# Kernel optimization log

Measured on AMD Instinct MI355X. Metric: run time of the kernel, lower is better.

## Reference

```python
import jax, jax.numpy as jnp
from jax import lax
import numpy as np

B, S, T = 512, 1024, 64  # batch, seq_len, tag_vocab_size


def setup_inputs() -> dict:
    key = jax.random.key(0)
    k1, k2, k3, k4 = jax.random.split(key, 4)
    tags = jax.random.randint(k1, (B, S), 0, T)
    # sequences sorted by length descending, as the original slicing scheme assumes
    lengths = jnp.sort(jax.random.randint(k2, (B,), 1, S + 1))[::-1]
    mask = jnp.arange(S)[None, :] < lengths[:, None]  # [B,S] bool
    emit_score = jax.random.normal(k3, (B, S, T), dtype=jnp.float32)
    transition = jax.random.normal(k4, (T, T), dtype=jnp.float32)
    return {"tags": tags, "mask": mask, "emit_score": emit_score, "transition": transition}


def reference(tags, mask, emit_score, transition):
    maskf = mask.astype(emit_score.dtype)
    # gold-path score: emission at gold tags + transition between consecutive gold tags
    score = jnp.take_along_axis(emit_score, tags[:, :, None], axis=2)[..., 0]  # [B,S]
    score = score.at[:, 1:].add(transition[tags[:, :-1], tags[:, 1:]])
    total_score = (score * maskf).sum(axis=1)  # [B]

    # forward algorithm (logsumexp-semiring scan over time)
    def step(d, inputs):
        emit_i, mask_i = inputs  # [B,T], [B]
        # log_sum[b, t_prev, t_cur] = d[b,t_prev] + transition[t_prev,t_cur] + emit_i[b,t_cur]
        cand = jax.nn.logsumexp(d[:, :, None] + transition[None, :, :] + emit_i[:, None, :], axis=1)
        d = jnp.where(mask_i[:, None], cand, d)  # finished sequences keep their alpha
        return d, None

    d0 = emit_score[:, 0]  # [B,T]
    emits_t = jnp.swapaxes(emit_score, 0, 1)[1:]  # [S-1,B,T]
    masks_t = mask.T[1:]  # [S-1,B]
    d, _ = lax.scan(step, d0, (emits_t, masks_t))
    log_z = jax.nn.logsumexp(d, axis=1)  # [B]
    return -(total_score - log_z)
```

## Files before the change

### kernel.cpp

```cpp
#include <hip/hip_runtime.h>
#include <stdint.h>

#define NB 512
#define SL 1024
#define NT 64

typedef float v4f __attribute__((ext_vector_type(4)));

__device__ __forceinline__ float wave_max6(float v) {
    #pragma unroll
    for (int off = 32; off >= 1; off >>= 1)
        v = fmaxf(v, __shfl_xor(v, off, 64));
    return v;
}
__device__ __forceinline__ float wave_sum_f(float v) {
    #pragma unroll
    for (int off = 32; off >= 1; off >>= 1)
        v += __shfl_xor(v, off, 64);
    return v;
}

__device__ __forceinline__ uint32_t bf16_rne(float x) {
    uint32_t u = __float_as_uint(x);
    return (u + 0x7fffu + ((u >> 16) & 1u)) >> 16;
}

__device__ __forceinline__ void dot2bf(float& acc, uint32_t a, uint32_t b) {
    asm("v_dot2_f32_bf16 %0, %1, %2, %0" : "+v"(acc) : "v"(a), "v"(b));
}

__global__ void __launch_bounds__(64) crf_fused_kernel(
    const int* __restrict__ tags, const void* __restrict__ mask,
    const float* __restrict__ emit, const float* __restrict__ trans,
    float* __restrict__ out)
{
    const int b = blockIdx.x;
    const int lane = threadIdx.x;
    const float* erow = emit + (size_t)b * SL * NT;
    const int* trow = tags + b * SL;

    const unsigned char* mb = (const unsigned char*)mask;
    const bool mask_is_i32 = ((mb[1] | mb[2] | mb[3]) == 0);

    float acc = 0.f; int cnt = 0;
    #pragma unroll
    for (int j = 0; j < 16; ++j) {
        const int i = lane + 64 * j;
        const int mk = mask_is_i32 ? (((const int*)mask)[(size_t)b * SL + i] != 0)
                                   : (mb[(size_t)b * SL + i] != 0);
        if (mk) {
            const int tg = trow[i];
            float val = erow[(size_t)i * NT + tg];
            if (i > 0) val += trans[trow[i - 1] * NT + tg];
            acc += val; cnt += 1;
        }
    }
    #pragma unroll
    for (int off = 32; off >= 1; off >>= 1) {
        acc += __shfl_xor(acc, off, 64);
        cnt += __shfl_xor(cnt, off, 64);
    }
    const float ts = acc;
    const int len = cnt;

    uint32_t Epk[NT / 2];
    #pragma unroll
    for (int m = 0; m < NT / 2; ++m) {
        uint32_t lo = bf16_rne(__expf(trans[(2 * m + 0) * NT + lane]));
        uint32_t hi = bf16_rne(__expf(trans[(2 * m + 1) * NT + lane]));
        Epk[m] = lo | (hi << 16);
    }

    __shared__ __align__(16) uint16_t vbuf16[NT];

    float d0 = erow[lane];
    float m0 = wave_max6(d0);
    float v = __expf(d0 - m0);
    float logacc = m0;

#define STEP(EX)                                                           \
    {                                                                      \
        vbuf16[lane] = (uint16_t)bf16_rne(v);                              \
        __builtin_amdgcn_wave_barrier();                                   \
        float a0 = 0.f, a1 = 0.f, a2 = 0.f, a3 = 0.f;                      \
        float a4 = 0.f, a5 = 0.f, a6 = 0.f, a7 = 0.f;                      \
        const uint4* vb = (const uint4*)vbuf16;                            \
        _Pragma("unroll")                                                  \
        for (int r = 0; r < 8; r += 2) {                                   \
            uint4 q0 = vb[r];                                              \
            uint4 q1 = vb[r + 1];                                          \
            dot2bf(a0, q0.x, Epk[4 * r + 0]);                              \
            dot2bf(a1, q0.y, Epk[4 * r + 1]);                              \
            dot2bf(a2, q0.z, Epk[4 * r + 2]);                              \
            dot2bf(a3, q0.w, Epk[4 * r + 3]);                              \
            dot2bf(a4, q1.x, Epk[4 * r + 4]);                              \
            dot2bf(a5, q1.y, Epk[4 * r + 5]);                              \
            dot2bf(a6, q1.z, Epk[4 * r + 6]);                              \
            dot2bf(a7, q1.w, Epk[4 * r + 7]);                              \
        }                                                                  \
        float h = ((a0 + a1) + (a2 + a3)) + ((a4 + a5) + (a6 + a7));       \
        v = h * (EX);                                                      \
    }

    const int nstep = len - 1;
    const int ngrp = nstep >> 2;
    int i = 1;

    v4f emq;
    if (ngrp > 0) {
        emq.x = erow[(i + 0) * NT + lane];
        emq.y = erow[(i + 1) * NT + lane];
        emq.z = erow[(i + 2) * NT + lane];
        emq.w = erow[(i + 3) * NT + lane];
    }
    for (int g = 0; g < ngrp; ++g) {
        float ex0 = __expf(emq.x), ex1 = __expf(emq.y);
        float ex2 = __expf(emq.z), ex3 = __expf(emq.w);
        const int ip = i + 4;
        if (g + 1 < ngrp) {
            emq.x = erow[(ip + 0) * NT + lane];
            emq.y = erow[(ip + 1) * NT + lane];
            emq.z = erow[(ip + 2) * NT + lane];
            emq.w = erow[(ip + 3) * NT + lane];
        }
        STEP(ex0)
        STEP(ex1)
        STEP(ex2)
        STEP(ex3)
        {
            uint32_t sb = __builtin_amdgcn_readfirstlane(__float_as_uint(v));
            int ex = (int)((sb >> 23) & 0xffu);
            v *= __uint_as_float((uint32_t)(254 - ex) << 23);
            logacc += (float)(ex - 127) * 0.69314718055994530942f;
        }
        i += 4;
    }
    for (; i < len; ++i) {
        float e = __expf(erow[i * NT + lane]);
        STEP(e)
    }
#undef STEP

    float sum = wave_sum_f(v);
    float log_z = logacc + __logf(sum);
    if (lane == 0) out[b] = -(ts - log_z);
}

extern "C" void kernel_launch(void* const* d_in, const int* in_sizes, int n_in,
                              void* d_out, int out_size, void* d_ws, size_t ws_size,
                              hipStream_t stream) {
    (void)in_sizes; (void)n_in; (void)out_size; (void)d_ws; (void)ws_size;
    const int*   tags  = (const int*)d_in[0];
    const void*  mask  = d_in[1];
    const float* emit  = (const float*)d_in[2];
    const float* trans = (const float*)d_in[3];
    float* out = (float*)d_out;

    crf_fused_kernel<<<dim3(NB), dim3(64), 0, stream>>>(tags, mask, emit, trans, out);
}
```

Baseline: 388.8 us.

## Replace LDS broadcast of alpha vector with DPP row rotations and bpermute

```diff
diff --git a/kernel.cpp b/kernel.cpp
--- a/kernel.cpp
+++ b/kernel.cpp
@@ -27,6 +27,30 @@
 
 __device__ __forceinline__ void dot2bf(float& acc, uint32_t a, uint32_t b) {
     asm("v_dot2_f32_bf16 %0, %1, %2, %0" : "+v"(acc) : "v"(a), "v"(b));
+}
+__device__ __forceinline__ float dot2bf3(uint32_t a, uint32_t b, float c) {
+    float d;
+    asm("v_dot2_f32_bf16 %0, %1, %2, %3" : "=v"(d) : "v"(a), "v"(b), "v"(c));
+    return d;
+}
+
+__device__ __forceinline__ uint32_t cvtpk_bf16(float lo, float hi) {
+    uint32_t r;
+    asm("v_cvt_pk_bf16_f32 %0, %1, %2" : "=v"(r) : "v"(lo), "v"(hi));
+    return r;
+}
+
+#define ROR1 0x121
+#define ROR2 0x122
+#define ROR4 0x124
+#define ROR8 0x128
+template <int CTRL>
+__device__ __forceinline__ uint32_t dpp_u(uint32_t x) {
+    return (uint32_t)__builtin_amdgcn_mov_dpp((int)x, CTRL, 0xf, 0xf, true);
+}
+
+__device__ __forceinline__ float bperm_f(int addr, float x) {
+    return __int_as_float(__builtin_amdgcn_ds_bpermute(addr, __float_as_int(x)));
 }
 
 __global__ void __launch_bounds__(64) crf_fused_kernel(
@@ -63,43 +87,80 @@
     const float ts = acc;
     const int len = cnt;
 
-    uint32_t Epk[NT / 2];
-    #pragma unroll
-    for (int m = 0; m < NT / 2; ++m) {
-        uint32_t lo = bf16_rne(__expf(trans[(2 * m + 0) * NT + lane]));
-        uint32_t hi = bf16_rne(__expf(trans[(2 * m + 1) * NT + lane]));
-        Epk[m] = lo | (hi << 16);
-    }
-
-    __shared__ __align__(16) uint16_t vbuf16[NT];
+    uint32_t idx = (uint32_t)lane;
+    uint32_t i1 = dpp_u<ROR1>(idx);
+    uint32_t wIdx[8];
+    wIdx[0] = idx | (i1 << 16);
+    wIdx[1] = dpp_u<ROR2>(wIdx[0]);
+    wIdx[2] = dpp_u<ROR4>(wIdx[0]);
+    wIdx[3] = dpp_u<ROR4>(wIdx[1]);
+    wIdx[4] = dpp_u<ROR8>(wIdx[0]);
+    wIdx[5] = dpp_u<ROR8>(wIdx[1]);
+    wIdx[6] = dpp_u<ROR8>(wIdx[2]);
+    wIdx[7] = dpp_u<ROR8>(wIdx[3]);
+
+    uint32_t EpkR[4][8];
+    #pragma unroll
+    for (int k = 0; k < 4; ++k) {
+        const int col = lane ^ (k << 4);
+        #pragma unroll
+        for (int j = 0; j < 8; ++j) {
+            const int lo = (int)(wIdx[j] & 0xffffu);
+            const int hi = (int)(wIdx[j] >> 16);
+            const uint32_t el = bf16_rne(__expf(trans[lo * NT + col]));
+            const uint32_t eh = bf16_rne(__expf(trans[hi * NT + col]));
+            EpkR[k][j] = el | (eh << 16);
+        }
+    }
+
+    const int a16 = (lane ^ 16) << 2;
+    const int a32 = (lane ^ 32) << 2;
+    const int a48 = (lane ^ 48) << 2;
+    const float fzero = 0.0f;
 
     float d0 = erow[lane];
     float m0 = wave_max6(d0);
     float v = __expf(d0 - m0);
     float logacc = m0;
 
-#define STEP(EX)                                                           \
-    {                                                                      \
-        vbuf16[lane] = (uint16_t)bf16_rne(v);                              \
-        __builtin_amdgcn_wave_barrier();                                   \
-        float a0 = 0.f, a1 = 0.f, a2 = 0.f, a3 = 0.f;                      \
-        float a4 = 0.f, a5 = 0.f, a6 = 0.f, a7 = 0.f;                      \
-        const uint4* vb = (const uint4*)vbuf16;                            \
-        _Pragma("unroll")                                                  \
-        for (int r = 0; r < 8; r += 2) {                                   \
-            uint4 q0 = vb[r];                                              \
-            uint4 q1 = vb[r + 1];                                          \
-            dot2bf(a0, q0.x, Epk[4 * r + 0]);                              \
-            dot2bf(a1, q0.y, Epk[4 * r + 1]);                              \
-            dot2bf(a2, q0.z, Epk[4 * r + 2]);                              \
-            dot2bf(a3, q0.w, Epk[4 * r + 3]);                              \
-            dot2bf(a4, q1.x, Epk[4 * r + 4]);                              \
-            dot2bf(a5, q1.y, Epk[4 * r + 5]);                              \
-            dot2bf(a6, q1.z, Epk[4 * r + 6]);                              \
-            dot2bf(a7, q1.w, Epk[4 * r + 7]);                              \
-        }                                                                  \
-        float h = ((a0 + a1) + (a2 + a3)) + ((a4 + a5) + (a6 + a7));       \
-        v = h * (EX);                                                      \
+#define STEP(EX)                                                            \
+    {                                                                       \
+        const uint32_t n1 = dpp_u<ROR1>(__float_as_uint(v));                \
+        const uint32_t w0 = cvtpk_bf16(v, __uint_as_float(n1));             \
+        const uint32_t w1 = dpp_u<ROR2>(w0);                                \
+        const uint32_t w2 = dpp_u<ROR4>(w0);                                \
+        const uint32_t w3 = dpp_u<ROR4>(w1);                                \
+        const uint32_t w4 = dpp_u<ROR8>(w0);                                \
+        const uint32_t w5 = dpp_u<ROR8>(w1);                                \
+        const uint32_t w6 = dpp_u<ROR8>(w2);                                \
+        const uint32_t w7 = dpp_u<ROR8>(w3);                                \
+        float a0 = dot2bf3(w0, EpkR[0][0], fzero);                          \
+        float a1 = dot2bf3(w0, EpkR[1][0], fzero);                          \
+        float a2 = dot2bf3(w0, EpkR[2][0], fzero);                          \
+        float a3 = dot2bf3(w0, EpkR[3][0], fzero);                          \
+        dot2bf(a0, w1, EpkR[0][1]); dot2bf(a1, w1, EpkR[1][1]);             \
+        dot2bf(a2, w1, EpkR[2][1]); dot2bf(a3, w1, EpkR[3][1]);             \
+        dot2bf(a0, w2, EpkR[0][2]); dot2bf(a1, w2, EpkR[1][2]);             \
+        dot2bf(a2, w2, EpkR[2][2]); dot2bf(a3, w2, EpkR[3][2]);             \
+        dot2bf(a0, w3, EpkR[0][3]); dot2bf(a1, w3, EpkR[1][3]);             \
+        dot2bf(a2, w3, EpkR[2][3]); dot2bf(a3, w3, EpkR[3][3]);             \
+        float b0 = dot2bf3(w4, EpkR[0][4], fzero);                          \
+        float b1 = dot2bf3(w4, EpkR[1][4], fzero);                          \
+        float b2 = dot2bf3(w4, EpkR[2][4], fzero);                          \
+        float b3 = dot2bf3(w4, EpkR[3][4], fzero);                          \
+        dot2bf(b0, w5, EpkR[0][5]); dot2bf(b1, w5, EpkR[1][5]);             \
+        dot2bf(b2, w5, EpkR[2][5]); dot2bf(b3, w5, EpkR[3][5]);             \
+        dot2bf(b0, w6, EpkR[0][6]); dot2bf(b1, w6, EpkR[1][6]);             \
+        dot2bf(b2, w6, EpkR[2][6]); dot2bf(b3, w6, EpkR[3][6]);             \
+        dot2bf(b0, w7, EpkR[0][7]); dot2bf(b1, w7, EpkR[1][7]);             \
+        dot2bf(b2, w7, EpkR[2][7]); dot2bf(b3, w7, EpkR[3][7]);             \
+        const float acc1 = a1 + b1;                                         \
+        const float acc2 = a2 + b2;                                         \
+        const float acc3 = a3 + b3;                                         \
+        const float x1 = bperm_f(a16, acc1);                                \
+        const float x2 = bperm_f(a32, acc2);                                \
+        const float x3 = bperm_f(a48, acc3);                                \
+        v = (((a0 + b0) + x1) + (x2 + x3)) * (EX);                          \
     }
 
     const int nstep = len - 1;
```

New measurement: 359.2 us. -7.6%, faster.

## Batch 16 sequences per wave and run forward recursion with MFMA

Applied to the files above, without the earlier changes.

```diff
diff --git a/kernel.cpp b/kernel.cpp
--- a/kernel.cpp
+++ b/kernel.cpp
@@ -4,146 +4,214 @@
 #define NB 512
 #define SL 1024
 #define NT 64
-
-typedef float v4f __attribute__((ext_vector_type(4)));
-
-__device__ __forceinline__ float wave_max6(float v) {
-    #pragma unroll
-    for (int off = 32; off >= 1; off >>= 1)
-        v = fmaxf(v, __shfl_xor(v, off, 64));
-    return v;
-}
-__device__ __forceinline__ float wave_sum_f(float v) {
-    #pragma unroll
-    for (int off = 32; off >= 1; off >>= 1)
-        v += __shfl_xor(v, off, 64);
-    return v;
-}
+#define BPB 16
+
+typedef __attribute__((ext_vector_type(8))) short bf16x8;
+typedef __attribute__((ext_vector_type(4))) float f32x4;
+typedef __attribute__((ext_vector_type(4))) unsigned int u32x4;
 
 __device__ __forceinline__ uint32_t bf16_rne(float x) {
     uint32_t u = __float_as_uint(x);
     return (u + 0x7fffu + ((u >> 16) & 1u)) >> 16;
 }
-
-__device__ __forceinline__ void dot2bf(float& acc, uint32_t a, uint32_t b) {
-    asm("v_dot2_f32_bf16 %0, %1, %2, %0" : "+v"(acc) : "v"(a), "v"(b));
-}
-
-__global__ void __launch_bounds__(64) crf_fused_kernel(
+__device__ __forceinline__ uint32_t cvtpk_bf16(float lo, float hi) {
+    uint32_t r;
+    asm("v_cvt_pk_bf16_f32 %0, %1, %2" : "=v"(r) : "v"(lo), "v"(hi));
+    return r;
+}
+__device__ __forceinline__ void plswap16_f(float& a, float& b) {
+    asm("v_permlane16_swap_b32 %0, %1" : "+v"(a), "+v"(b));
+}
+__device__ __forceinline__ void plswap32_f(float& a, float& b) {
+    asm("v_permlane32_swap_b32 %0, %1" : "+v"(a), "+v"(b));
+}
+__device__ __forceinline__ void plswap16_i(int& a, int& b) {
+    asm("v_permlane16_swap_b32 %0, %1" : "+v"(a), "+v"(b));
+}
+__device__ __forceinline__ void plswap32_i(int& a, int& b) {
+    asm("v_permlane32_swap_b32 %0, %1" : "+v"(a), "+v"(b));
+}
+
+__device__ __forceinline__ f32x4 mfma_bf16(const u32x4& a, const u32x4& b, const f32x4& c) {
+    union U { u32x4 u; bf16x8 s; };
+    U ua; ua.u = a;
+    U ub; ub.u = b;
+    return __builtin_amdgcn_mfma_f32_16x16x32_bf16(ua.s, ub.s, c, 0, 0, 0);
+}
+
+__global__ void __launch_bounds__(64) crf_mfma_kernel(
     const int* __restrict__ tags, const void* __restrict__ mask,
     const float* __restrict__ emit, const float* __restrict__ trans,
     float* __restrict__ out)
 {
-    const int b = blockIdx.x;
+    const int b0 = blockIdx.x * BPB;
     const int lane = threadIdx.x;
-    const float* erow = emit + (size_t)b * SL * NT;
-    const int* trow = tags + b * SL;
+    const int q = lane >> 4;
+    const int n = lane & 15;
+    const int bb = b0 + n;
+
+    const int* trow = tags + (size_t)bb * SL;
+    const float* erow = emit + (size_t)bb * SL * NT;
 
     const unsigned char* mb = (const unsigned char*)mask;
-    const bool mask_is_i32 = ((mb[1] | mb[2] | mb[3]) == 0);
-
-    float acc = 0.f; int cnt = 0;
+    const bool m32 = ((mb[1] | mb[2] | mb[3]) == 0);
+
+    float acc = 0.f;
+    int cnt = 0;
+    const int i0 = q * (SL / 4);
+    #pragma unroll 8
+    for (int jj = 0; jj < SL / 4; ++jj) {
+        const int i = i0 + jj;
+        const int mk = m32 ? (((const int*)mask)[(size_t)bb * SL + i] != 0)
+                           : (mb[(size_t)bb * SL + i] != 0);
+        const int tg = trow[i];
+        float val = erow[(size_t)i * NT + tg];
+        if (i > 0) val += trans[trow[i - 1] * NT + tg];
+        acc += mk ? val : 0.f;
+        cnt += mk;
+    }
+    {
+        float pa = acc, pb = acc;
+        plswap16_f(pa, pb); acc = pa + pb;
+        pa = acc; pb = acc;
+        plswap32_f(pa, pb); acc = pa + pb;
+        int ca = cnt, cb = cnt;
+        plswap16_i(ca, cb); cnt = ca + cb;
+        ca = cnt; cb = cnt;
+        plswap32_i(ca, cb); cnt = ca + cb;
+    }
+    const float tsn = acc;
+    const int fin = cnt - 1;
+    const int lmax = __shfl(cnt, 0, 64);
+    const int last = lmax - 1;
+
+    u32x4 Afr[4][2];
     #pragma unroll
-    for (int j = 0; j < 16; ++j) {
-        const int i = lane + 64 * j;
-        const int mk = mask_is_i32 ? (((const int*)mask)[(size_t)b * SL + i] != 0)
-                                   : (mb[(size_t)b * SL + i] != 0);
-        if (mk) {
-            const int tg = trow[i];
-            float val = erow[(size_t)i * NT + tg];
-            if (i > 0) val += trans[trow[i - 1] * NT + tg];
-            acc += val; cnt += 1;
-        }
-    }
+    for (int T = 0; T < 4; ++T) {
+        #pragma unroll
+        for (int kt = 0; kt < 2; ++kt) {
+            uint32_t wv[4];
+            #pragma unroll
+            for (int w = 0; w < 4; ++w) {
+                const int p0 = 16 * (2 * kt + (w >> 1)) + 4 * q + 2 * (w & 1);
+                const int m = 16 * T + n;
+                const uint32_t lo = bf16_rne(__expf(trans[p0 * NT + m]));
+                const uint32_t hi = bf16_rne(__expf(trans[(p0 + 1) * NT + m]));
+                wv[w] = lo | (hi << 16);
+            }
+            Afr[T][kt].x = wv[0]; Afr[T][kt].y = wv[1];
+            Afr[T][kt].z = wv[2]; Afr[T][kt].w = wv[3];
+        }
+    }
+
+    const float* ep = erow + 4 * q;
+    f32x4 d[4];
     #pragma unroll
-    for (int off = 32; off >= 1; off >>= 1) {
-        acc += __shfl_xor(acc, off, 64);
-        cnt += __shfl_xor(cnt, off, 64);
-    }
-    const float ts = acc;
-    const int len = cnt;
-
-    uint32_t Epk[NT / 2];
-    #pragma unroll
-    for (int m = 0; m < NT / 2; ++m) {
-        uint32_t lo = bf16_rne(__expf(trans[(2 * m + 0) * NT + lane]));
-        uint32_t hi = bf16_rne(__expf(trans[(2 * m + 1) * NT + lane]));
-        Epk[m] = lo | (hi << 16);
-    }
-
-    __shared__ __align__(16) uint16_t vbuf16[NT];
-
-    float d0 = erow[lane];
-    float m0 = wave_max6(d0);
-    float v = __expf(d0 - m0);
-    float logacc = m0;
-
-#define STEP(EX)                                                           \
-    {                                                                      \
-        vbuf16[lane] = (uint16_t)bf16_rne(v);                              \
-        __builtin_amdgcn_wave_barrier();                                   \
-        float a0 = 0.f, a1 = 0.f, a2 = 0.f, a3 = 0.f;                      \
-        float a4 = 0.f, a5 = 0.f, a6 = 0.f, a7 = 0.f;                      \
-        const uint4* vb = (const uint4*)vbuf16;                            \
-        _Pragma("unroll")                                                  \
-        for (int r = 0; r < 8; r += 2) {                                   \
-            uint4 q0 = vb[r];                                              \
-            uint4 q1 = vb[r + 1];                                          \
-            dot2bf(a0, q0.x, Epk[4 * r + 0]);                              \
-            dot2bf(a1, q0.y, Epk[4 * r + 1]);                              \
-            dot2bf(a2, q0.z, Epk[4 * r + 2]);                              \
-            dot2bf(a3, q0.w, Epk[4 * r + 3]);                              \
-            dot2bf(a4, q1.x, Epk[4 * r + 4]);                              \
-            dot2bf(a5, q1.y, Epk[4 * r + 5]);                              \
-            dot2bf(a6, q1.z, Epk[4 * r + 6]);                              \
-            dot2bf(a7, q1.w, Epk[4 * r + 7]);                              \
-        }                                                                  \
-        float h = ((a0 + a1) + (a2 + a3)) + ((a4 + a5) + (a6 + a7));       \
-        v = h * (EX);                                                      \
-    }
-
-    const int nstep = len - 1;
-    const int ngrp = nstep >> 2;
+    for (int T = 0; T < 4; ++T) {
+        f32x4 e = *(const f32x4*)(ep + 16 * T);
+        d[T].x = __expf(e.x); d[T].y = __expf(e.y);
+        d[T].z = __expf(e.z); d[T].w = __expf(e.w);
+    }
+    float logacc = 0.f;
+
+    auto extractNow = [&](int icur) {
+        f32x4 s4 = d[0] + d[1] + d[2] + d[3];
+        float sl = (s4.x + s4.y) + (s4.z + s4.w);
+        float pa = sl, pb = sl;
+        plswap16_f(pa, pb); sl = pa + pb;
+        pa = sl; pb = sl;
+        plswap32_f(pa, pb); sl = pa + pb;
+        if (q == 0 && fin == icur)
+            out[bb] = -(tsn - (logacc + __logf(sl)));
+    };
+
+    auto step = [&](const f32x4 (&et)[4]) {
+        f32x4 ex[4];
+        #pragma unroll
+        for (int T = 0; T < 4; ++T) {
+            ex[T].x = __expf(et[T].x); ex[T].y = __expf(et[T].y);
+            ex[T].z = __expf(et[T].z); ex[T].w = __expf(et[T].w);
+        }
+        u32x4 B0, B1;
+        B0.x = cvtpk_bf16(d[0].x, d[0].y); B0.y = cvtpk_bf16(d[0].z, d[0].w);
+        B0.z = cvtpk_bf16(d[1].x, d[1].y); B0.w = cvtpk_bf16(d[1].z, d[1].w);
+        B1.x = cvtpk_bf16(d[2].x, d[2].y); B1.y = cvtpk_bf16(d[2].z, d[2].w);
+        B1.z = cvtpk_bf16(d[3].x, d[3].y); B1.w = cvtpk_bf16(d[3].z, d[3].w);
+        const f32x4 z = {0.f, 0.f, 0.f, 0.f};
+        #pragma unroll
+        for (int T = 0; T < 4; ++T) {
+            f32x4 a = mfma_bf16(Afr[T][0], B0, z);
+            a = mfma_bf16(Afr[T][1], B1, a);
+            d[T] = a * ex[T];
+        }
+    };
+
+    auto renorm = [&]() {
+        float rep = d[0].x;
+        float pa = rep, pb = rep;
+        plswap16_f(pa, pb); rep = fmaxf(pa, pb);
+        pa = rep; pb = rep;
+        plswap32_f(pa, pb); rep = fmaxf(pa, pb);
+        const uint32_t ub = __float_as_uint(rep);
+        const int e = (int)((ub >> 23) & 255u);
+        const float sc = __uint_as_float((uint32_t)(254 - e) << 23);
+        #pragma unroll
+        for (int T = 0; T < 4; ++T) d[T] *= sc;
+        logacc += (float)(e - 127) * 0.69314718055994530942f;
+    };
+
+    auto loadGroup = [&](f32x4 (&buf)[4][4], int i) {
+        #pragma unroll
+        for (int s = 0; s < 4; ++s) {
+            int r = i + s;
+            r = r < last ? r : last;
+            #pragma unroll
+            for (int T = 0; T < 4; ++T)
+                buf[s][T] = *(const f32x4*)(ep + (size_t)r * NT + 16 * T);
+        }
+    };
+
+    auto doGroup = [&](const f32x4 (&buf)[4][4], int i) {
+        const bool gate = (__ballot((fin >= i) && (fin <= i + 3)) != 0ULL);
+        #pragma unroll
+        for (int s = 0; s < 4; ++s) {
+            step(buf[s]);
+            if (gate) {
+                if (__ballot(fin == i + s) != 0ULL) extractNow(i + s);
+            }
+        }
+        renorm();
+    };
+
+    if (__ballot(fin == 0) != 0ULL) extractNow(0);
+
     int i = 1;
-
-    v4f emq;
-    if (ngrp > 0) {
-        emq.x = erow[(i + 0) * NT + lane];
-        emq.y = erow[(i + 1) * NT + lane];
-        emq.z = erow[(i + 2) * NT + lane];
-        emq.w = erow[(i + 3) * NT + lane];
-    }
-    for (int g = 0; g < ngrp; ++g) {
-        float ex0 = __expf(emq.x), ex1 = __expf(emq.y);
-        float ex2 = __expf(emq.z), ex3 = __expf(emq.w);
-        const int ip = i + 4;
-        if (g + 1 < ngrp) {
-            emq.x = erow[(ip + 0) * NT + lane];
-            emq.y = erow[(ip + 1) * NT + lane];
-            emq.z = erow[(ip + 2) * NT + lane];
-            emq.w = erow[(ip + 3) * NT + lane];
-        }
-        STEP(ex0)
-        STEP(ex1)
-        STEP(ex2)
-        STEP(ex3)
-        {
-            uint32_t sb = __builtin_amdgcn_readfirstlane(__float_as_uint(v));
-            int ex = (int)((sb >> 23) & 0xffu);
-            v *= __uint_as_float((uint32_t)(254 - ex) << 23);
-            logacc += (float)(ex - 127) * 0.69314718055994530942f;
-        }
-        i += 4;
-    }
-    for (; i < len; ++i) {
-        float e = __expf(erow[i * NT + lane]);
-        STEP(e)
-    }
-#undef STEP
-
-    float sum = wave_sum_f(v);
-    float log_z = logacc + __logf(sum);
-    if (lane == 0) out[b] = -(ts - log_z);
+    if (last >= 1) {
+        f32x4 eA[4][4], eB[4][4];
+        if (i + 3 <= last) {
+            loadGroup(eA, i);
+            for (;;) {
+                const bool more = (i + 7 <= last);
+                if (more) loadGroup(eB, i + 4);
+                doGroup(eA, i);
+                i += 4;
+                if (!more) break;
+                const bool more2 = (i + 7 <= last);
+                if (more2) loadGroup(eA, i + 4);
+                doGroup(eB, i);
+                i += 4;
+                if (!more2) break;
+            }
+        }
+        for (; i <= last; ++i) {
+            f32x4 er[4];
+            #pragma unroll
+            for (int T = 0; T < 4; ++T)
+                er[T] = *(const f32x4*)(ep + (size_t)i * NT + 16 * T);
+            step(er);
+            if (__ballot(fin == i) != 0ULL) extractNow(i);
+        }
+    }
 }
 
 extern "C" void kernel_launch(void* const* d_in, const int* in_sizes, int n_in,
@@ -156,5 +224,5 @@
     const float* trans = (const float*)d_in[3];
     float* out = (float*)d_out;
 
-    crf_fused_kernel<<<dim3(NB), dim3(64), 0, stream>>>(tags, mask, emit, trans, out);
-}
+    crf_mfma_kernel<<<dim3(NB / BPB), dim3(64), 0, stream>>>(tags, mask, emit, trans, out);
+}
```

Result: slower. 661.1 us (+70.1%).
